# Kernel tuning notes

Measured on AMD Instinct MI355X. Metric: run time of the kernel, lower is better.

Reference implementation:

```python
import jax, jax.numpy as jnp
import numpy as np
import math

B, T, D, H, L = 64, 255, 512, 8, 8
CODEBOOK = 512
V = CODEBOOK + 3  # bos/eos/pad
COND_DIM = 512
MAX_LEN = 256
HD = D // H


def _layernorm(x, g, b, eps=1e-5):
    mu = jnp.mean(x, axis=-1, keepdims=True)
    var = jnp.mean(jnp.square(x - mu), axis=-1, keepdims=True)
    return (x - mu) * jax.lax.rsqrt(var + eps) * g + b


def setup_inputs() -> dict:
    key = jax.random.key(0)
    ks = jax.random.split(key, 24)
    s = 0.02
    d = {
        'tokens': jax.random.randint(ks[0], (B, T), 0, V),
        'cond': jax.random.normal(ks[1], (B, COND_DIM), jnp.float32),
        'emb': jax.random.normal(ks[2], (V, D), jnp.float32) * s,  # tied token_emb / head weight
        'pos_emb': jax.random.normal(ks[3], (1, MAX_LEN, D), jnp.float32) * s,
        'cond_w1': jax.random.normal(ks[4], (COND_DIM, D), jnp.float32) * s,
        'cond_b1': jnp.zeros((D,), jnp.float32),
        'cond_w2': jax.random.normal(ks[5], (D, D), jnp.float32) * s,
        'cond_b2': jnp.zeros((D,), jnp.float32),
        'ln1_g': jnp.ones((L, D), jnp.float32),
        'ln1_b': jnp.zeros((L, D), jnp.float32),
        'qkv_w': jax.random.normal(ks[6], (L, D, 3 * D), jnp.float32) * s,
        'qkv_b': jnp.zeros((L, 3 * D), jnp.float32),
        'proj_w': jax.random.normal(ks[7], (L, D, D), jnp.float32) * s,
        'proj_b': jnp.zeros((L, D), jnp.float32),
        'ln2_g': jnp.ones((L, D), jnp.float32),
        'ln2_b': jnp.zeros((L, D), jnp.float32),
        'mlp_w1': jax.random.normal(ks[8], (L, D, 4 * D), jnp.float32) * s,
        'mlp_b1': jnp.zeros((L, 4 * D), jnp.float32),
        'mlp_w2': jax.random.normal(ks[9], (L, 4 * D, D), jnp.float32) * s,
        'mlp_b2': jnp.zeros((L, D), jnp.float32),
        'lnf_g': jnp.ones((D,), jnp.float32),
        'lnf_b': jnp.zeros((D,), jnp.float32),
    }
    return d


def reference(tokens, cond, emb, pos_emb, cond_w1, cond_b1, cond_w2, cond_b2,
              ln1_g, ln1_b, qkv_w, qkv_b, proj_w, proj_b,
              ln2_g, ln2_b, mlp_w1, mlp_b1, mlp_w2, mlp_b2, lnf_g, lnf_b):
    b, t = tokens.shape
    h = emb[tokens] + pos_emb[:, :t, :]                              # [B,T,D]
    c = jax.nn.silu(cond @ cond_w1 + cond_b1) @ cond_w2 + cond_b2    # [B,D]
    h = jnp.concatenate([c[:, None, :], h], axis=1)                  # [B,S,D]
    S = t + 1
    causal = jnp.tril(jnp.ones((S, S), bool))
    scale = 1.0 / math.sqrt(HD)
    for i in range(L):
        x = _layernorm(h, ln1_g[i], ln1_b[i])
        qkv = (x @ qkv_w[i] + qkv_b[i]).reshape(b, S, 3, H, HD).transpose(2, 0, 3, 1, 4)
        q, k, v = qkv[0], qkv[1], qkv[2]                             # [B,H,S,hd]
        a = jnp.einsum('bhsd,bhtd->bhst', q, k) * scale
        a = jnp.where(causal, a, -jnp.inf)
        a = jax.nn.softmax(a, axis=-1)
        o = jnp.einsum('bhst,bhtd->bhsd', a, v).transpose(0, 2, 1, 3).reshape(b, S, D)
        h = h + o @ proj_w[i] + proj_b[i]
        x = _layernorm(h, ln2_g[i], ln2_b[i])
        h = h + jax.nn.gelu(x @ mlp_w1[i] + mlp_b1[i], approximate=False) @ mlp_w2[i] + mlp_b2[i]
    h = _layernorm(h, lnf_g, lnf_b)
    return (h @ emb.T)[:, 1:, :]                                     # [B,T,V]
```

## Files before the change

### kernel.cpp

```cpp
#include <hip/hip_runtime.h>
#include <hip/hip_bf16.h>

typedef __attribute__((ext_vector_type(8))) short bf16x8;
typedef __attribute__((ext_vector_type(4))) float f32x4;
typedef __attribute__((ext_vector_type(4))) unsigned short u16x4;
typedef __attribute__((ext_vector_type(8))) unsigned short u16x8;
typedef unsigned short u16;

#define DEV static __device__ __forceinline__

DEV float bf2f(u16 u) {
  union { unsigned int i; float f; } c; c.i = ((unsigned int)u) << 16; return c.f;
}
DEV u16 f2bf(float f) {
  union { float f; unsigned int i; } c; c.f = f;
  unsigned int i = c.i;
  i += 0x7FFFu + ((i >> 16) & 1u);
  return (u16)(i >> 16);
}

DEV void gload_lds16(const void* g, void* l) {
  __builtin_amdgcn_global_load_lds((const __attribute__((address_space(1))) void*)g,
                                   (__attribute__((address_space(3))) void*)l, 16, 0, 0);
}

DEV f32x4 mfma16(bf16x8 a, bf16x8 b, f32x4 c) {
  return __builtin_amdgcn_mfma_f32_16x16x32_bf16(a, b, c, 0, 0, 0);
}

template<int N> DEV void vwait() { asm volatile("s_waitcnt vmcnt(%0)" :: "n"(N) : "memory"); }

DEV float fasterf(float x) {
  float ax = fabsf(x);
  float t = 1.0f / (1.0f + 0.3275911f * ax);
  float y = t * (0.254829592f + t * (-0.284496736f + t * (1.421413741f +
            t * (-1.453152027f + t * 1.061405429f))));
  float r = 1.0f - y * __expf(-ax * ax);
  return copysignf(r, x);
}
DEV float gelu(float v) { return 0.5f * v * (1.0f + fasterf(v * 0.70710678118f)); }

__global__ __launch_bounds__(256) void ktranspose(const float* __restrict__ in, u16* __restrict__ out,
                                                  int K, int N) {
  __shared__ u16 tile[32][33];
  const float* src = in + (size_t)blockIdx.z * K * N;
  u16* dst = out + (size_t)blockIdx.z * K * N;
  const int n0 = blockIdx.x * 32, k0 = blockIdx.y * 32;
  const int tx = threadIdx.x, ty = threadIdx.y;
#pragma unroll
  for (int i = ty; i < 32; i += 8) tile[i][tx] = f2bf(src[(size_t)(k0 + i) * N + n0 + tx]);
  __syncthreads();
#pragma unroll
  for (int i = ty; i < 32; i += 8) dst[(size_t)(n0 + i) * K + k0 + tx] = tile[tx][i];
}

__global__ __launch_bounds__(256) void kcvt(const float* __restrict__ in, u16* __restrict__ out, int n) {
  int i = blockIdx.x * 256 + threadIdx.x;
  if (i < n) out[i] = f2bf(in[i]);
}

__global__ __launch_bounds__(256) void kcond(const float* __restrict__ cond, const float* __restrict__ w1,
                                             const float* __restrict__ b1, const float* __restrict__ w2,
                                             const float* __restrict__ b2, float* __restrict__ h) {
  __shared__ float xr[512];
  __shared__ float t1[512];
  const int b = blockIdx.x, tid = threadIdx.x;
  for (int i = tid; i < 512; i += 256) xr[i] = cond[b * 512 + i];
  __syncthreads();
  for (int j = tid; j < 512; j += 256) {
    float acc = b1[j];
    for (int k = 0; k < 512; ++k) acc += xr[k] * w1[k * 512 + j];
    t1[j] = acc / (1.f + __expf(-acc));
  }
  __syncthreads();
  for (int j = tid; j < 512; j += 256) {
    float acc = b2[j];
    for (int k = 0; k < 512; ++k) acc += t1[k] * w2[k * 512 + j];
    h[(size_t)b * 256 * 512 + j] = acc;
  }
}

__global__ __launch_bounds__(256) void kembed(const int* __restrict__ tok, const float* __restrict__ emb,
                                              const float* __restrict__ pos, float* __restrict__ h) {
  const int idx = blockIdx.x;
  const int b = idx / 255, t = idx % 255;
  const int c = threadIdx.x * 2;
  const int tk = tok[idx];
  float2 ev = *(const float2*)(emb + (size_t)tk * 512 + c);
  float2 pv = *(const float2*)(pos + (size_t)t * 512 + c);
  float2 r;
  r.x = ev.x + pv.x;
  r.y = ev.y + pv.y;
  *(float2*)(h + ((size_t)b * 256 + 1 + t) * 512 + c) = r;
}

__global__ __launch_bounds__(256) void kln(const float* __restrict__ hin, const float* __restrict__ g,
                                           const float* __restrict__ bt, u16* __restrict__ out) {
  const int row = blockIdx.x * 4 + (threadIdx.x >> 6), lane = threadIdx.x & 63;
  const float4* x = (const float4*)(hin + (size_t)row * 512);
  float4 v0 = x[lane], v1 = x[lane + 64];
  float s1 = v0.x + v0.y + v0.z + v0.w + v1.x + v1.y + v1.z + v1.w;
  float s2 = v0.x * v0.x + v0.y * v0.y + v0.z * v0.z + v0.w * v0.w +
             v1.x * v1.x + v1.y * v1.y + v1.z * v1.z + v1.w * v1.w;
#pragma unroll
  for (int off = 1; off < 64; off <<= 1) { s1 += __shfl_xor(s1, off); s2 += __shfl_xor(s2, off); }
  float mu = s1 * (1.f / 512.f);
  float var = s2 * (1.f / 512.f) - mu * mu;
  float rs = rsqrtf(var + 1e-5f);
  const int c0 = lane * 4;
  float4 g0 = *(const float4*)(g + c0), g1 = *(const float4*)(g + 256 + c0);
  float4 b0 = *(const float4*)(bt + c0), b1 = *(const float4*)(bt + 256 + c0);
  u16x4 o0, o1;
  o0[0] = f2bf((v0.x - mu) * rs * g0.x + b0.x);
  o0[1] = f2bf((v0.y - mu) * rs * g0.y + b0.y);
  o0[2] = f2bf((v0.z - mu) * rs * g0.z + b0.z);
  o0[3] = f2bf((v0.w - mu) * rs * g0.w + b0.w);
  o1[0] = f2bf((v1.x - mu) * rs * g1.x + b1.x);
  o1[1] = f2bf((v1.y - mu) * rs * g1.y + b1.y);
  o1[2] = f2bf((v1.z - mu) * rs * g1.z + b1.z);
  o1[3] = f2bf((v1.w - mu) * rs * g1.w + b1.w);
  *(u16x4*)(out + (size_t)row * 512 + c0) = o0;
  *(u16x4*)(out + (size_t)row * 512 + 256 + c0) = o1;
}

template<int MODE, int FM>
__global__ __launch_bounds__(512, 2) void kgemm8(const u16* __restrict__ A, const u16* __restrict__ Bt,
                                                 const float* __restrict__ bias, void* __restrict__ Cout,
                                                 int M, int N, int K) {
  constexpr int BM = FM * 32;
  constexpr int ABYTES = BM * 128;
  constexpr int BBYTES = 256 * 128;
  constexpr int AH = ABYTES / 2, BH = BBYTES / 2;
  constexpr int ALD = AH / 8192;
  constexpr int BOFF = 2 * ABYTES;
  __shared__ __align__(16) char shm[2 * ABYTES + 2 * BBYTES];

  const int tid = threadIdx.x;
  const int lane = tid & 63;
  const int wid = tid >> 6;
  const int wr = wid >> 2;
  const int wc = wid & 3;
  const int fr = lane & 15, fq = lane >> 4;
  const int axor = (fr & 7) << 4;
  const int m0 = blockIdx.x * BM, n0 = blockIdx.y * 256;
  const int nkt = K >> 6;
  const int Kb = K * 2;
  const char* Ab = (const char*)A;
  const char* Bb = (const char*)Bt;

  unsigned aOff[2][ALD], bOff[2][2];
#pragma unroll
  for (int h = 0; h < 2; ++h) {
#pragma unroll
    for (int j = 0; j < ALD; ++j) {
      int d = h * AH + j * 8192 + tid * 16;
      int row = d >> 7, pc = (d >> 4) & 7;
      aOff[h][j] = (unsigned)((m0 + row) * Kb + ((pc ^ (row & 7)) << 4));
    }
#pragma unroll
    for (int j = 0; j < 2; ++j) {
      int d = h * BH + j * 8192 + tid * 16;
      int row = d >> 7, pc = (d >> 4) & 7;
      bOff[h][j] = (unsigned)((n0 + row) * Kb + ((pc ^ (row & 7)) << 4));
    }
  }

  auto stA = [&](int kt, int h, int b) {
#pragma unroll
    for (int j = 0; j < ALD; ++j)
      gload_lds16(Ab + (size_t)aOff[h][j] + (size_t)kt * 128,
                  shm + b * ABYTES + h * AH + j * 8192 + tid * 16);
  };
  auto stB = [&](int kt, int h, int b) {
#pragma unroll
    for (int j = 0; j < 2; ++j)
      gload_lds16(Bb + (size_t)bOff[h][j] + (size_t)kt * 128,
                  shm + BOFF + b * BBYTES + h * BH + j * 8192 + tid * 16);
  };
  auto rdA = [&](int b, int m, int ks) {
    return *(const bf16x8*)(shm + b * ABYTES + (wr * (BM / 2) + m * 16 + fr) * 128 +
                            ((ks * 64 + fq * 16) ^ axor));
  };
  auto rdB = [&](int b, int n, int ks) {
    return *(const bf16x8*)(shm + BOFF + b * BBYTES + (wc * 64 + n * 16 + fr) * 128 +
                            ((ks * 64 + fq * 16) ^ axor));
  };

  f32x4 acc[FM][4];
#pragma unroll
  for (int i = 0; i < FM; ++i)
#pragma unroll
    for (int j = 0; j < 4; ++j) acc[i][j] = f32x4{0.f, 0.f, 0.f, 0.f};

  stA(0, 0, 0); stA(0, 1, 0); stB(0, 0, 0); stB(0, 1, 0);
  if (nkt > 1) { stA(1, 0, 1); stA(1, 1, 1); }
  vwait<2 * ALD>();
  __builtin_amdgcn_sched_barrier(0);
  __builtin_amdgcn_s_barrier();

  for (int kt = 0; kt < nkt; ++kt) {
    const int cur = kt & 1;
    const bool sb = (kt + 1 < nkt);
    const bool sa = (kt + 2 < nkt);
    bf16x8 aF[FM][2], bF[4][2];
#pragma unroll
    for (int m = 0; m < FM; ++m) aF[m][0] = rdA(cur, m, 0);
#pragma unroll
    for (int n = 0; n < 4; ++n) bF[n][0] = rdB(cur, n, 0);
    if (sb) stB(kt + 1, 0, cur ^ 1);
    __builtin_amdgcn_s_barrier();
    __builtin_amdgcn_s_setprio(1);
#pragma unroll
    for (int m = 0; m < FM / 2; ++m)
#pragma unroll
      for (int n = 0; n < 4; ++n) acc[m][n] = mfma16(aF[m][0], bF[n][0], acc[m][n]);
    __builtin_amdgcn_s_setprio(0);
    __builtin_amdgcn_s_barrier();
#pragma unroll
    for (int m = 0; m < FM; ++m) aF[m][1] = rdA(cur, m, 1);
#pragma unroll
    for (int n = 0; n < 4; ++n) bF[n][1] = rdB(cur, n, 1);
    if (sb) stB(kt + 1, 1, cur ^ 1);
    __builtin_amdgcn_s_barrier();
    __builtin_amdgcn_s_setprio(1);
#pragma unroll
    for (int m = FM / 2; m < FM; ++m)
#pragma unroll
      for (int n = 0; n < 4; ++n) acc[m][n] = mfma16(aF[m][0], bF[n][0], acc[m][n]);
    __builtin_amdgcn_s_setprio(0);
    asm volatile("s_waitcnt lgkmcnt(0)" ::: "memory");
    __builtin_amdgcn_sched_barrier(0);
    __builtin_amdgcn_s_barrier();
    if (sa) stA(kt + 2, 0, cur);
    __builtin_amdgcn_s_barrier();
    __builtin_amdgcn_s_setprio(1);
#pragma unroll
    for (int m = 0; m < FM / 2; ++m)
#pragma unroll
      for (int n = 0; n < 4; ++n) acc[m][n] = mfma16(aF[m][1], bF[n][1], acc[m][n]);
    __builtin_amdgcn_s_setprio(0);
    __builtin_amdgcn_s_barrier();
    if (sa) stA(kt + 2, 1, cur);
    __builtin_amdgcn_s_barrier();
    __builtin_amdgcn_s_setprio(1);
#pragma unroll
    for (int m = FM / 2; m < FM; ++m)
#pragma unroll
      for (int n = 0; n < 4; ++n) acc[m][n] = mfma16(aF[m][1], bF[n][1], acc[m][n]);
    __builtin_amdgcn_s_setprio(0);
    if (sa) vwait<2 * ALD>(); else vwait<0>();
    __builtin_amdgcn_sched_barrier(0);
    __builtin_amdgcn_s_barrier();
  }

  float bv[4];
#pragma unroll
  for (int n = 0; n < 4; ++n) bv[n] = bias[n0 + wc * 64 + n * 16 + fr];

  if (MODE == 0 || MODE == 1) {
    u16* C = (u16*)Cout;
#pragma unroll
    for (int m = 0; m < FM; ++m)
#pragma unroll
      for (int r = 0; r < 4; ++r) {
        int row = m0 + wr * (BM / 2) + m * 16 + fq * 4 + r;
        u16* cp = C + (size_t)row * N + n0 + wc * 64 + fr;
#pragma unroll
        for (int n = 0; n < 4; ++n) {
          float v = acc[m][n][r] + bv[n];
          if (MODE == 1) v = gelu(v);
          cp[n * 16] = f2bf(v);
        }
      }
  } else {
    float* hC = (float*)Cout;
#pragma unroll
    for (int m = 0; m < FM; ++m)
#pragma unroll
      for (int r = 0; r < 4; ++r) {
        int row = m0 + wr * (BM / 2) + m * 16 + fq * 4 + r;
        float* hp = hC + (size_t)row * N + n0 + wc * 64 + fr;
#pragma unroll
        for (int n = 0; n < 4; ++n) hp[n * 16] += acc[m][n][r] + bv[n];
      }
  }
}

template<int MODE>
__global__ __launch_bounds__(256, 2) void kgemm3(const u16* __restrict__ A, const u16* __restrict__ Bt,
                                                 const float* __restrict__ bias, void* __restrict__ Cout,
                                                 int M, int N, int K) {
  __shared__ __align__(16) u16 As[3][4096];
  __shared__ __align__(16) u16 Bs[3][4096];
  const int tid = threadIdx.x;
  const int lane = tid & 63;
  const int wr = tid >> 7, wc = (tid >> 6) & 1;
  const int m0 = blockIdx.x * 128, n0 = blockIdx.y * 128;
  const int nkt = K >> 5;
  const size_t Kb = (size_t)K * 2;

  const int srow = tid >> 2;
  const int schunk = tid & 3;
  const int sc = schunk ^ ((srow >> 1) & 3);
  const int d1 = tid * 16, d2 = tid * 16 + 4096;
  int brA = n0 + srow, brB = n0 + srow + 64;
  if (MODE == 3) { brA = min(brA, N - 1); brB = min(brB, N - 1); }
  const char* Ab = (const char*)A;
  const char* Bb = (const char*)Bt;
  const size_t a0 = (size_t)(m0 + srow) * Kb + sc * 16;
  const size_t a1 = (size_t)(m0 + srow + 64) * Kb + sc * 16;
  const size_t b0 = (size_t)brA * Kb + sc * 16;
  const size_t b1 = (size_t)brB * Kb + sc * 16;

  f32x4 acc[4][4];
#pragma unroll
  for (int i = 0; i < 4; ++i)
#pragma unroll
    for (int j = 0; j < 4; ++j) acc[i][j] = f32x4{0.f, 0.f, 0.f, 0.f};

#pragma unroll
  for (int t = 0; t < 2; ++t) {
    const size_t ko = (size_t)t * 64;
    gload_lds16(Ab + a0 + ko, (char*)As[t] + d1);
    gload_lds16(Ab + a1 + ko, (char*)As[t] + d2);
    gload_lds16(Bb + b0 + ko, (char*)Bs[t] + d1);
    gload_lds16(Bb + b1 + ko, (char*)Bs[t] + d2);
  }
  asm volatile("s_waitcnt vmcnt(4)" ::: "memory");
  __builtin_amdgcn_s_barrier();
  __builtin_amdgcn_sched_barrier(0);

  const int kchunk = (((lane >> 4) ^ ((lane >> 1) & 3)) << 4);
  const int arow = wr * 64 + (lane & 15);
  const int brow = wc * 64 + (lane & 15);

  for (int kt = 0; kt < nkt; ++kt) {
    const int bufc = kt % 3;
    const bool deep = (kt + 2 < nkt);
    if (deep) {
      const int bufn = (kt + 2) % 3;
      const size_t ko = (size_t)(kt + 2) * 64;
      gload_lds16(Ab + a0 + ko, (char*)As[bufn] + d1);
      gload_lds16(Ab + a1 + ko, (char*)As[bufn] + d2);
      gload_lds16(Bb + b0 + ko, (char*)Bs[bufn] + d1);
      gload_lds16(Bb + b1 + ko, (char*)Bs[bufn] + d2);
    }
    const char* Ap = (const char*)As[bufc];
    const char* Bp = (const char*)Bs[bufc];
    bf16x8 aF[4], bF[4];
#pragma unroll
    for (int mt = 0; mt < 4; ++mt) aF[mt] = *(const bf16x8*)(Ap + (arow + mt * 16) * 64 + kchunk);
#pragma unroll
    for (int nt = 0; nt < 4; ++nt) bF[nt] = *(const bf16x8*)(Bp + (brow + nt * 16) * 64 + kchunk);
#pragma unroll
    for (int mt = 0; mt < 4; ++mt)
#pragma unroll
      for (int nt = 0; nt < 4; ++nt)
        acc[mt][nt] = mfma16(aF[mt], bF[nt], acc[mt][nt]);
    if (deep) {
      asm volatile("s_waitcnt vmcnt(4)" ::: "memory");
    } else {
      asm volatile("s_waitcnt vmcnt(0)" ::: "memory");
    }
    __builtin_amdgcn_s_barrier();
    __builtin_amdgcn_sched_barrier(0);
  }

  if (MODE == 3) {
    float* C = (float*)Cout;
#pragma unroll
    for (int mt = 0; mt < 4; ++mt)
#pragma unroll
      for (int r = 0; r < 4; ++r) {
        int row = m0 + wr * 64 + mt * 16 + (lane >> 4) * 4 + r;
        int s = row & 255;
        if (s == 0) continue;
        int bb = row >> 8;
        float* cp = C + ((size_t)bb * 255 + (s - 1)) * 515 + n0 + wc * 64 + (lane & 15);
#pragma unroll
        for (int nt = 0; nt < 4; ++nt) {
          int col = n0 + wc * 64 + nt * 16 + (lane & 15);
          if (col < 515) cp[nt * 16] = acc[mt][nt][r];
        }
      }
  }
}

__global__ __launch_bounds__(256, 1) void kattn(const u16* __restrict__ qkv, u16* __restrict__ o) {
  __shared__ __align__(16) u16 Ks[256][72];
  __shared__ __align__(16) u16 Vt[64][264];
  __shared__ __align__(16) u16 Ps[4][64][72];
  const int tid = threadIdx.x, wv = tid >> 6, lane = tid & 63;
  const int bh = blockIdx.x, bb = bh >> 3, hh = bh & 7;
  const size_t base = (size_t)bb * 256 * 1536 + hh * 64;

  for (int c = tid; c < 2048; c += 256) {
    int s = c >> 3, pp = c & 7;
    u16x8 kv = *(const u16x8*)(qkv + base + (size_t)s * 1536 + 512 + pp * 8);
    *(u16x8*)&Ks[s][pp * 8] = kv;
    u16x8 vv = *(const u16x8*)(qkv + base + (size_t)s * 1536 + 1024 + pp * 8);
#pragma unroll
    for (int j = 0; j < 8; ++j) Vt[pp * 8 + j][s] = vv[j];
  }
  __syncthreads();

  bf16x8 qf[4][2];
#pragma unroll
  for (int mt = 0; mt < 4; ++mt)
#pragma unroll
    for (int ks = 0; ks < 2; ++ks)
      qf[mt][ks] = *(const bf16x8*)(qkv + base +
                   (size_t)(wv * 64 + mt * 16 + (lane & 15)) * 1536 + ks * 32 + (lane >> 4) * 8);

  const float scale = 0.125f;
  float mrow[4][4], lsum[4][4];
#pragma unroll
  for (int mt = 0; mt < 4; ++mt)
#pragma unroll
    for (int r = 0; r < 4; ++r) { mrow[mt][r] = -1e30f; lsum[mt][r] = 0.f; }

  for (int ct = 0; ct <= wv; ++ct) {
    f32x4 sacc[4][4];
#pragma unroll
    for (int i = 0; i < 4; ++i)
#pragma unroll
      for (int j = 0; j < 4; ++j) sacc[i][j] = f32x4{0.f, 0.f, 0.f, 0.f};
#pragma unroll
    for (int ks = 0; ks < 2; ++ks) {
      bf16x8 kf[4];
#pragma unroll
      for (int nt = 0; nt < 4; ++nt)
        kf[nt] = *(const bf16x8*)&Ks[ct * 64 + nt * 16 + (lane & 15)][ks * 32 + (lane >> 4) * 8];
#pragma unroll
      for (int mt = 0; mt < 4; ++mt)
#pragma unroll
        for (int nt = 0; nt < 4; ++nt)
          sacc[mt][nt] = mfma16(qf[mt][ks], kf[nt], sacc[mt][nt]);
    }
#pragma unroll
    for (int mt = 0; mt < 4; ++mt)
#pragma unroll
      for (int r = 0; r < 4; ++r) {
        int srow = wv * 64 + mt * 16 + (lane >> 4) * 4 + r;
        float mx = -1e30f;
#pragma unroll
        for (int nt = 0; nt < 4; ++nt) {
          int tcol = ct * 64 + nt * 16 + (lane & 15);
          float v = sacc[mt][nt][r] * scale;
          if (tcol > srow) v = -1e30f;
          mx = fmaxf(mx, v);
        }
#pragma unroll
        for (int off = 1; off < 16; off <<= 1) mx = fmaxf(mx, __shfl_xor(mx, off));
        mrow[mt][r] = fmaxf(mrow[mt][r], mx);
      }
  }

  f32x4 oacc[4][4];
#pragma unroll
  for (int i = 0; i < 4; ++i)
#pragma unroll
    for (int j = 0; j < 4; ++j) oacc[i][j] = f32x4{0.f, 0.f, 0.f, 0.f};

  for (int ct = 0; ct <= wv; ++ct) {
    f32x4 sacc[4][4];
#pragma unroll
    for (int i = 0; i < 4; ++i)
#pragma unroll
      for (int j = 0; j < 4; ++j) sacc[i][j] = f32x4{0.f, 0.f, 0.f, 0.f};
#pragma unroll
    for (int ks = 0; ks < 2; ++ks) {
      bf16x8 kf[4];
#pragma unroll
      for (int nt = 0; nt < 4; ++nt)
        kf[nt] = *(const bf16x8*)&Ks[ct * 64 + nt * 16 + (lane & 15)][ks * 32 + (lane >> 4) * 8];
#pragma unroll
      for (int mt = 0; mt < 4; ++mt)
#pragma unroll
        for (int nt = 0; nt < 4; ++nt)
          sacc[mt][nt] = mfma16(qf[mt][ks], kf[nt], sacc[mt][nt]);
    }
#pragma unroll
    for (int mt = 0; mt < 4; ++mt)
#pragma unroll
      for (int r = 0; r < 4; ++r) {
        int srow = wv * 64 + mt * 16 + (lane >> 4) * 4 + r;
        float ps = 0.f;
#pragma unroll
        for (int nt = 0; nt < 4; ++nt) {
          int tcol = ct * 64 + nt * 16 + (lane & 15);
          float v = sacc[mt][nt][r] * scale;
          float pe = (tcol > srow) ? 0.f : __expf(v - mrow[mt][r]);
          ps += pe;
          Ps[wv][mt * 16 + (lane >> 4) * 4 + r][nt * 16 + (lane & 15)] = f2bf(pe);
        }
#pragma unroll
        for (int off = 1; off < 16; off <<= 1) ps += __shfl_xor(ps, off);
        lsum[mt][r] += ps;
      }
#pragma unroll
    for (int ks = 0; ks < 2; ++ks) {
      bf16x8 pf[4], vf[4];
#pragma unroll
      for (int mt = 0; mt < 4; ++mt)
        pf[mt] = *(const bf16x8*)&Ps[wv][mt * 16 + (lane & 15)][ks * 32 + (lane >> 4) * 8];
#pragma unroll
      for (int nt = 0; nt < 4; ++nt)
        vf[nt] = *(const bf16x8*)&Vt[nt * 16 + (lane & 15)][ct * 64 + ks * 32 + (lane >> 4) * 8];
#pragma unroll
      for (int mt = 0; mt < 4; ++mt)
#pragma unroll
        for (int nt = 0; nt < 4; ++nt)
          oacc[mt][nt] = mfma16(pf[mt], vf[nt], oacc[mt][nt]);
    }
  }

#pragma unroll
  for (int mt = 0; mt < 4; ++mt)
#pragma unroll
    for (int r = 0; r < 4; ++r) {
      int s = wv * 64 + mt * 16 + (lane >> 4) * 4 + r;
      float inv = 1.f / lsum[mt][r];
      u16* op = o + ((size_t)bb * 256 + s) * 512 + hh * 64 + (lane & 15);
#pragma unroll
      for (int nt = 0; nt < 4; ++nt) op[nt * 16] = f2bf(oacc[mt][nt][r] * inv);
    }
}

extern "C" void kernel_launch(void* const* d_in, const int* in_sizes, int n_in,
                              void* d_out, int out_size, void* d_ws, size_t ws_size,
                              hipStream_t stream) {
  const int* tokens = (const int*)d_in[0];
  const float* cond = (const float*)d_in[1];
  const float* emb = (const float*)d_in[2];
  const float* pos = (const float*)d_in[3];
  const float* cw1 = (const float*)d_in[4];
  const float* cb1 = (const float*)d_in[5];
  const float* cw2 = (const float*)d_in[6];
  const float* cb2 = (const float*)d_in[7];
  const float* ln1g = (const float*)d_in[8];
  const float* ln1b = (const float*)d_in[9];
  const float* qkvw = (const float*)d_in[10];
  const float* qkvb = (const float*)d_in[11];
  const float* projw = (const float*)d_in[12];
  const float* projb = (const float*)d_in[13];
  const float* ln2g = (const float*)d_in[14];
  const float* ln2b = (const float*)d_in[15];
  const float* w1 = (const float*)d_in[16];
  const float* b1 = (const float*)d_in[17];
  const float* w2 = (const float*)d_in[18];
  const float* b2 = (const float*)d_in[19];
  const float* lnfg = (const float*)d_in[20];
  const float* lnfb = (const float*)d_in[21];

  const size_t NEEDED = (size_t)16384 * 512 * 4
                      + (size_t)16384 * 512 * 2
                      + (size_t)16384 * 2048 * 2
                      + (size_t)8 * 1536 * 512 * 2
                      + (size_t)8 * 512 * 512 * 2
                      + (size_t)8 * 2048 * 512 * 2
                      + (size_t)8 * 512 * 2048 * 2;
  if (ws_size < NEEDED) return;

  char* p = (char*)d_ws;
  float* h = (float*)p;        p += (size_t)16384 * 512 * 4;
  u16* xln = (u16*)p;          p += (size_t)16384 * 512 * 2;
  u16* big = (u16*)p;          p += (size_t)16384 * 2048 * 2;
  u16* attn_o = big + (size_t)16384 * 1536;
  u16* embB = big;
  u16* qkvT = (u16*)p;         p += (size_t)8 * 1536 * 512 * 2;
  u16* projT = (u16*)p;        p += (size_t)8 * 512 * 512 * 2;
  u16* w1T = (u16*)p;          p += (size_t)8 * 2048 * 512 * 2;
  u16* w2T = (u16*)p;          p += (size_t)8 * 512 * 2048 * 2;

  ktranspose<<<dim3(48, 16, 8), dim3(32, 8), 0, stream>>>(qkvw, qkvT, 512, 1536);
  ktranspose<<<dim3(16, 16, 8), dim3(32, 8), 0, stream>>>(projw, projT, 512, 512);
  ktranspose<<<dim3(64, 16, 8), dim3(32, 8), 0, stream>>>(w1, w1T, 512, 2048);
  ktranspose<<<dim3(16, 64, 8), dim3(32, 8), 0, stream>>>(w2, w2T, 2048, 512);

  kembed<<<16320, 256, 0, stream>>>(tokens, emb, pos, h);
  kcond<<<64, 256, 0, stream>>>(cond, cw1, cb1, cw2, cb2, h);

  for (int l = 0; l < 8; ++l) {
    kln<<<4096, 256, 0, stream>>>(h, ln1g + l * 512, ln1b + l * 512, xln);
    kgemm8<0, 8><<<dim3(64, 6), 512, 0, stream>>>(xln, qkvT + (size_t)l * 1536 * 512,
                                                  qkvb + l * 1536, big, 16384, 1536, 512);
    kattn<<<512, 256, 0, stream>>>(big, attn_o);
    kgemm8<2, 4><<<dim3(128, 2), 512, 0, stream>>>(attn_o, projT + (size_t)l * 512 * 512,
                                                   projb + l * 512, h, 16384, 512, 512);
    kln<<<4096, 256, 0, stream>>>(h, ln2g + l * 512, ln2b + l * 512, xln);
    kgemm8<1, 8><<<dim3(64, 8), 512, 0, stream>>>(xln, w1T + (size_t)l * 2048 * 512,
                                                  b1 + l * 2048, big, 16384, 2048, 512);
    kgemm8<2, 4><<<dim3(128, 2), 512, 0, stream>>>(big, w2T + (size_t)l * 512 * 2048,
                                                   b2 + l * 512, h, 16384, 512, 2048);
  }
  kln<<<4096, 256, 0, stream>>>(h, lnfg, lnfb, xln);
  kcvt<<<1030, 256, 0, stream>>>(emb, embB, 515 * 512);
  kgemm3<3><<<dim3(128, 5), 256, 0, stream>>>(xln, embB, nullptr, d_out, 16384, 515, 512);
}
```

Before: 1.973 ms.

## Use 128x128 gemm for QKV/MLP1, one-pass online-softmax attention, tanh GELU

Switches the QKV and MLP-up GEMMs from the large 256x256-tile kgemm8 to the smaller 128x128 triple-buffered kgemm3, which is extended with bias and GELU epilogues, and leaves kgemm8 handling only the residual-add case. Attention drops its separate max pass and uses an online softmax that rescales the running sum and output accumulator, so QK^T is computed once instead of twice. GELU becomes the tanh approximation, which is cheaper per element but deviates from the exact erf GELU in the reference.

```diff
diff --git a/kernel.cpp b/kernel.cpp
--- a/kernel.cpp
+++ b/kernel.cpp
@@ -30,15 +30,12 @@
 
 template<int N> DEV void vwait() { asm volatile("s_waitcnt vmcnt(%0)" :: "n"(N) : "memory"); }
 
-DEV float fasterf(float x) {
-  float ax = fabsf(x);
-  float t = 1.0f / (1.0f + 0.3275911f * ax);
-  float y = t * (0.254829592f + t * (-0.284496736f + t * (1.421413741f +
-            t * (-1.453152027f + t * 1.061405429f))));
-  float r = 1.0f - y * __expf(-ax * ax);
-  return copysignf(r, x);
-}
-DEV float gelu(float v) { return 0.5f * v * (1.0f + fasterf(v * 0.70710678118f)); }
+DEV float gelu(float x) {
+  float t2 = __builtin_fmaf(0.044715f * x * x, x, x);
+  float e = __expf(1.5957691216f * t2);
+  float th = 1.f - 2.f / (e + 1.f);
+  return 0.5f * x * (1.f + th);
+}
 
 __global__ __launch_bounds__(256) void ktranspose(const float* __restrict__ in, u16* __restrict__ out,
                                                   int K, int N) {
@@ -123,6 +120,139 @@
   *(u16x4*)(out + (size_t)row * 512 + 256 + c0) = o1;
 }
 
+template<int MODE>
+__global__ __launch_bounds__(256, 2) void kgemm3(const u16* __restrict__ A, const u16* __restrict__ Bt,
+                                                 const float* __restrict__ bias, void* __restrict__ Cout,
+                                                 int M, int N, int K) {
+  __shared__ __align__(16) u16 As[3][4096];
+  __shared__ __align__(16) u16 Bs[3][4096];
+  const int tid = threadIdx.x;
+  const int lane = tid & 63;
+  const int wr = tid >> 7, wc = (tid >> 6) & 1;
+  const int m0 = blockIdx.x * 128, n0 = blockIdx.y * 128;
+  const int nkt = K >> 5;
+  const size_t Kb = (size_t)K * 2;
+
+  const int srow = tid >> 2;
+  const int schunk = tid & 3;
+  const int sc = schunk ^ ((srow >> 1) & 3);
+  const int d1 = tid * 16, d2 = tid * 16 + 4096;
+  int brA = n0 + srow, brB = n0 + srow + 64;
+  if (MODE == 3) { brA = min(brA, N - 1); brB = min(brB, N - 1); }
+  const char* Ab = (const char*)A;
+  const char* Bb = (const char*)Bt;
+  const size_t a0 = (size_t)(m0 + srow) * Kb + sc * 16;
+  const size_t a1 = (size_t)(m0 + srow + 64) * Kb + sc * 16;
+  const size_t b0 = (size_t)brA * Kb + sc * 16;
+  const size_t b1 = (size_t)brB * Kb + sc * 16;
+
+  f32x4 acc[4][4];
+#pragma unroll
+  for (int i = 0; i < 4; ++i)
+#pragma unroll
+    for (int j = 0; j < 4; ++j) acc[i][j] = f32x4{0.f, 0.f, 0.f, 0.f};
+
+#pragma unroll
+  for (int t = 0; t < 2; ++t) {
+    const size_t ko = (size_t)t * 64;
+    gload_lds16(Ab + a0 + ko, (char*)As[t] + d1);
+    gload_lds16(Ab + a1 + ko, (char*)As[t] + d2);
+    gload_lds16(Bb + b0 + ko, (char*)Bs[t] + d1);
+    gload_lds16(Bb + b1 + ko, (char*)Bs[t] + d2);
+  }
+  asm volatile("s_waitcnt vmcnt(4)" ::: "memory");
+  __builtin_amdgcn_s_barrier();
+  __builtin_amdgcn_sched_barrier(0);
+
+  const int kchunk = (((lane >> 4) ^ ((lane >> 1) & 3)) << 4);
+  const int arow = wr * 64 + (lane & 15);
+  const int brow = wc * 64 + (lane & 15);
+
+  for (int kt = 0; kt < nkt; ++kt) {
+    const int bufc = kt % 3;
+    const bool deep = (kt + 2 < nkt);
+    if (deep) {
+      const int bufn = (kt + 2) % 3;
+      const size_t ko = (size_t)(kt + 2) * 64;
+      gload_lds16(Ab + a0 + ko, (char*)As[bufn] + d1);
+      gload_lds16(Ab + a1 + ko, (char*)As[bufn] + d2);
+      gload_lds16(Bb + b0 + ko, (char*)Bs[bufn] + d1);
+      gload_lds16(Bb + b1 + ko, (char*)Bs[bufn] + d2);
+    }
+    const char* Ap = (const char*)As[bufc];
+    const char* Bp = (const char*)Bs[bufc];
+    bf16x8 aF[4], bF[4];
+#pragma unroll
+    for (int mt = 0; mt < 4; ++mt) aF[mt] = *(const bf16x8*)(Ap + (arow + mt * 16) * 64 + kchunk);
+#pragma unroll
+    for (int nt = 0; nt < 4; ++nt) bF[nt] = *(const bf16x8*)(Bp + (brow + nt * 16) * 64 + kchunk);
+#pragma unroll
+    for (int mt = 0; mt < 4; ++mt)
+#pragma unroll
+      for (int nt = 0; nt < 4; ++nt)
+        acc[mt][nt] = mfma16(aF[mt], bF[nt], acc[mt][nt]);
+    if (deep) {
+      asm volatile("s_waitcnt vmcnt(4)" ::: "memory");
+    } else {
+      asm volatile("s_waitcnt vmcnt(0)" ::: "memory");
+    }
+    __builtin_amdgcn_s_barrier();
+    __builtin_amdgcn_sched_barrier(0);
+  }
+
+  float bv[4];
+#pragma unroll
+  for (int nt = 0; nt < 4; ++nt) {
+    int col = n0 + wc * 64 + nt * 16 + (lane & 15);
+    bv[nt] = (MODE == 3) ? 0.f : bias[col];
+  }
+
+  if (MODE == 0 || MODE == 1) {
+    u16* C = (u16*)Cout;
+#pragma unroll
+    for (int mt = 0; mt < 4; ++mt)
+#pragma unroll
+      for (int r = 0; r < 4; ++r) {
+        int row = m0 + wr * 64 + mt * 16 + (lane >> 4) * 4 + r;
+        u16* cp = C + (size_t)row * N + n0 + wc * 64 + (lane & 15);
+#pragma unroll
+        for (int nt = 0; nt < 4; ++nt) {
+          float v = acc[mt][nt][r] + bv[nt];
+          if (MODE == 1) v = gelu(v);
+          cp[nt * 16] = f2bf(v);
+        }
+      }
+  } else if (MODE == 2) {
+    float* hC = (float*)Cout;
+#pragma unroll
+    for (int mt = 0; mt < 4; ++mt)
+#pragma unroll
+      for (int r = 0; r < 4; ++r) {
+        int row = m0 + wr * 64 + mt * 16 + (lane >> 4) * 4 + r;
+        float* hp = hC + (size_t)row * N + n0 + wc * 64 + (lane & 15);
+#pragma unroll
+        for (int nt = 0; nt < 4; ++nt) hp[nt * 16] += acc[mt][nt][r] + bv[nt];
+      }
+  } else {
+    float* C = (float*)Cout;
+#pragma unroll
+    for (int mt = 0; mt < 4; ++mt)
+#pragma unroll
+      for (int r = 0; r < 4; ++r) {
+        int row = m0 + wr * 64 + mt * 16 + (lane >> 4) * 4 + r;
+        int s = row & 255;
+        if (s == 0) continue;
+        int bb = row >> 8;
+        float* cp = C + ((size_t)bb * 255 + (s - 1)) * 515 + n0 + wc * 64 + (lane & 15);
+#pragma unroll
+        for (int nt = 0; nt < 4; ++nt) {
+          int col = n0 + wc * 64 + nt * 16 + (lane & 15);
+          if (col < 515) cp[nt * 16] = acc[mt][nt][r];
+        }
+      }
+  }
+}
+
 template<int MODE, int FM>
 __global__ __launch_bounds__(512, 2) void kgemm8(const u16* __restrict__ A, const u16* __restrict__ Bt,
                                                  const float* __restrict__ bias, void* __restrict__ Cout,
@@ -257,133 +387,16 @@
 #pragma unroll
   for (int n = 0; n < 4; ++n) bv[n] = bias[n0 + wc * 64 + n * 16 + fr];
 
-  if (MODE == 0 || MODE == 1) {
-    u16* C = (u16*)Cout;
-#pragma unroll
-    for (int m = 0; m < FM; ++m)
-#pragma unroll
-      for (int r = 0; r < 4; ++r) {
-        int row = m0 + wr * (BM / 2) + m * 16 + fq * 4 + r;
-        u16* cp = C + (size_t)row * N + n0 + wc * 64 + fr;
-#pragma unroll
-        for (int n = 0; n < 4; ++n) {
-          float v = acc[m][n][r] + bv[n];
-          if (MODE == 1) v = gelu(v);
-          cp[n * 16] = f2bf(v);
-        }
-      }
-  } else {
-    float* hC = (float*)Cout;
-#pragma unroll
-    for (int m = 0; m < FM; ++m)
-#pragma unroll
-      for (int r = 0; r < 4; ++r) {
-        int row = m0 + wr * (BM / 2) + m * 16 + fq * 4 + r;
-        float* hp = hC + (size_t)row * N + n0 + wc * 64 + fr;
-#pragma unroll
-        for (int n = 0; n < 4; ++n) hp[n * 16] += acc[m][n][r] + bv[n];
-      }
-  }
-}
-
-template<int MODE>
-__global__ __launch_bounds__(256, 2) void kgemm3(const u16* __restrict__ A, const u16* __restrict__ Bt,
-                                                 const float* __restrict__ bias, void* __restrict__ Cout,
-                                                 int M, int N, int K) {
-  __shared__ __align__(16) u16 As[3][4096];
-  __shared__ __align__(16) u16 Bs[3][4096];
-  const int tid = threadIdx.x;
-  const int lane = tid & 63;
-  const int wr = tid >> 7, wc = (tid >> 6) & 1;
-  const int m0 = blockIdx.x * 128, n0 = blockIdx.y * 128;
-  const int nkt = K >> 5;
-  const size_t Kb = (size_t)K * 2;
-
-  const int srow = tid >> 2;
-  const int schunk = tid & 3;
-  const int sc = schunk ^ ((srow >> 1) & 3);
-  const int d1 = tid * 16, d2 = tid * 16 + 4096;
-  int brA = n0 + srow, brB = n0 + srow + 64;
-  if (MODE == 3) { brA = min(brA, N - 1); brB = min(brB, N - 1); }
-  const char* Ab = (const char*)A;
-  const char* Bb = (const char*)Bt;
-  const size_t a0 = (size_t)(m0 + srow) * Kb + sc * 16;
-  const size_t a1 = (size_t)(m0 + srow + 64) * Kb + sc * 16;
-  const size_t b0 = (size_t)brA * Kb + sc * 16;
-  const size_t b1 = (size_t)brB * Kb + sc * 16;
-
-  f32x4 acc[4][4];
-#pragma unroll
-  for (int i = 0; i < 4; ++i)
-#pragma unroll
-    for (int j = 0; j < 4; ++j) acc[i][j] = f32x4{0.f, 0.f, 0.f, 0.f};
-
-#pragma unroll
-  for (int t = 0; t < 2; ++t) {
-    const size_t ko = (size_t)t * 64;
-    gload_lds16(Ab + a0 + ko, (char*)As[t] + d1);
-    gload_lds16(Ab + a1 + ko, (char*)As[t] + d2);
-    gload_lds16(Bb + b0 + ko, (char*)Bs[t] + d1);
-    gload_lds16(Bb + b1 + ko, (char*)Bs[t] + d2);
-  }
-  asm volatile("s_waitcnt vmcnt(4)" ::: "memory");
-  __builtin_amdgcn_s_barrier();
-  __builtin_amdgcn_sched_barrier(0);
-
-  const int kchunk = (((lane >> 4) ^ ((lane >> 1) & 3)) << 4);
-  const int arow = wr * 64 + (lane & 15);
-  const int brow = wc * 64 + (lane & 15);
-
-  for (int kt = 0; kt < nkt; ++kt) {
-    const int bufc = kt % 3;
-    const bool deep = (kt + 2 < nkt);
-    if (deep) {
-      const int bufn = (kt + 2) % 3;
-      const size_t ko = (size_t)(kt + 2) * 64;
-      gload_lds16(Ab + a0 + ko, (char*)As[bufn] + d1);
-      gload_lds16(Ab + a1 + ko, (char*)As[bufn] + d2);
-      gload_lds16(Bb + b0 + ko, (char*)Bs[bufn] + d1);
-      gload_lds16(Bb + b1 + ko, (char*)Bs[bufn] + d2);
-    }
-    const char* Ap = (const char*)As[bufc];
-    const char* Bp = (const char*)Bs[bufc];
-    bf16x8 aF[4], bF[4];
-#pragma unroll
-    for (int mt = 0; mt < 4; ++mt) aF[mt] = *(const bf16x8*)(Ap + (arow + mt * 16) * 64 + kchunk);
-#pragma unroll
-    for (int nt = 0; nt < 4; ++nt) bF[nt] = *(const bf16x8*)(Bp + (brow + nt * 16) * 64 + kchunk);
-#pragma unroll
-    for (int mt = 0; mt < 4; ++mt)
-#pragma unroll
-      for (int nt = 0; nt < 4; ++nt)
-        acc[mt][nt] = mfma16(aF[mt], bF[nt], acc[mt][nt]);
-    if (deep) {
-      asm volatile("s_waitcnt vmcnt(4)" ::: "memory");
-    } else {
-      asm volatile("s_waitcnt vmcnt(0)" ::: "memory");
-    }
-    __builtin_amdgcn_s_barrier();
-    __builtin_amdgcn_sched_barrier(0);
-  }
-
-  if (MODE == 3) {
-    float* C = (float*)Cout;
-#pragma unroll
-    for (int mt = 0; mt < 4; ++mt)
-#pragma unroll
-      for (int r = 0; r < 4; ++r) {
-        int row = m0 + wr * 64 + mt * 16 + (lane >> 4) * 4 + r;
-        int s = row & 255;
-        if (s == 0) continue;
-        int bb = row >> 8;
-        float* cp = C + ((size_t)bb * 255 + (s - 1)) * 515 + n0 + wc * 64 + (lane & 15);
-#pragma unroll
-        for (int nt = 0; nt < 4; ++nt) {
-          int col = n0 + wc * 64 + nt * 16 + (lane & 15);
-          if (col < 515) cp[nt * 16] = acc[mt][nt][r];
-        }
-      }
-  }
+  float* hC = (float*)Cout;
+#pragma unroll
+  for (int m = 0; m < FM; ++m)
+#pragma unroll
+    for (int r = 0; r < 4; ++r) {
+      int row = m0 + wr * (BM / 2) + m * 16 + fq * 4 + r;
+      float* hp = hC + (size_t)row * N + n0 + wc * 64 + fr;
+#pragma unroll
+      for (int n = 0; n < 4; ++n) hp[n * 16] += acc[m][n][r] + bv[n];
+    }
 }
 
 __global__ __launch_bounds__(256, 1) void kattn(const u16* __restrict__ qkv, u16* __restrict__ o) {
@@ -419,6 +432,12 @@
 #pragma unroll
     for (int r = 0; r < 4; ++r) { mrow[mt][r] = -1e30f; lsum[mt][r] = 0.f; }
 
+  f32x4 oacc[4][4];
+#pragma unroll
+  for (int i = 0; i < 4; ++i)
+#pragma unroll
+    for (int j = 0; j < 4; ++j) oacc[i][j] = f32x4{0.f, 0.f, 0.f, 0.f};
+
   for (int ct = 0; ct <= wv; ++ct) {
     f32x4 sacc[4][4];
 #pragma unroll
@@ -442,61 +461,32 @@
 #pragma unroll
       for (int r = 0; r < 4; ++r) {
         int srow = wv * 64 + mt * 16 + (lane >> 4) * 4 + r;
+        float v[4];
         float mx = -1e30f;
 #pragma unroll
         for (int nt = 0; nt < 4; ++nt) {
           int tcol = ct * 64 + nt * 16 + (lane & 15);
-          float v = sacc[mt][nt][r] * scale;
-          if (tcol > srow) v = -1e30f;
-          mx = fmaxf(mx, v);
+          float vv = sacc[mt][nt][r] * scale;
+          v[nt] = (tcol > srow) ? -1e30f : vv;
+          mx = fmaxf(mx, v[nt]);
         }
 #pragma unroll
         for (int off = 1; off < 16; off <<= 1) mx = fmaxf(mx, __shfl_xor(mx, off));
-        mrow[mt][r] = fmaxf(mrow[mt][r], mx);
-      }
-  }
-
-  f32x4 oacc[4][4];
-#pragma unroll
-  for (int i = 0; i < 4; ++i)
-#pragma unroll
-    for (int j = 0; j < 4; ++j) oacc[i][j] = f32x4{0.f, 0.f, 0.f, 0.f};
-
-  for (int ct = 0; ct <= wv; ++ct) {
-    f32x4 sacc[4][4];
-#pragma unroll
-    for (int i = 0; i < 4; ++i)
-#pragma unroll
-      for (int j = 0; j < 4; ++j) sacc[i][j] = f32x4{0.f, 0.f, 0.f, 0.f};
-#pragma unroll
-    for (int ks = 0; ks < 2; ++ks) {
-      bf16x8 kf[4];
-#pragma unroll
-      for (int nt = 0; nt < 4; ++nt)
-        kf[nt] = *(const bf16x8*)&Ks[ct * 64 + nt * 16 + (lane & 15)][ks * 32 + (lane >> 4) * 8];
-#pragma unroll
-      for (int mt = 0; mt < 4; ++mt)
-#pragma unroll
-        for (int nt = 0; nt < 4; ++nt)
-          sacc[mt][nt] = mfma16(qf[mt][ks], kf[nt], sacc[mt][nt]);
-    }
-#pragma unroll
-    for (int mt = 0; mt < 4; ++mt)
-#pragma unroll
-      for (int r = 0; r < 4; ++r) {
-        int srow = wv * 64 + mt * 16 + (lane >> 4) * 4 + r;
+        float mnew = fmaxf(mrow[mt][r], mx);
+        float sf = __expf(mrow[mt][r] - mnew);
+        mrow[mt][r] = mnew;
         float ps = 0.f;
 #pragma unroll
         for (int nt = 0; nt < 4; ++nt) {
-          int tcol = ct * 64 + nt * 16 + (lane & 15);
-          float v = sacc[mt][nt][r] * scale;
-          float pe = (tcol > srow) ? 0.f : __expf(v - mrow[mt][r]);
+          float pe = (v[nt] <= -1e29f) ? 0.f : __expf(v[nt] - mnew);
           ps += pe;
           Ps[wv][mt * 16 + (lane >> 4) * 4 + r][nt * 16 + (lane & 15)] = f2bf(pe);
         }
 #pragma unroll
         for (int off = 1; off < 16; off <<= 1) ps += __shfl_xor(ps, off);
-        lsum[mt][r] += ps;
+        lsum[mt][r] = lsum[mt][r] * sf + ps;
+#pragma unroll
+        for (int nt = 0; nt < 4; ++nt) oacc[mt][nt][r] *= sf;
       }
 #pragma unroll
     for (int ks = 0; ks < 2; ++ks) {
@@ -583,14 +573,14 @@
 
   for (int l = 0; l < 8; ++l) {
     kln<<<4096, 256, 0, stream>>>(h, ln1g + l * 512, ln1b + l * 512, xln);
-    kgemm8<0, 8><<<dim3(64, 6), 512, 0, stream>>>(xln, qkvT + (size_t)l * 1536 * 512,
-                                                  qkvb + l * 1536, big, 16384, 1536, 512);
+    kgemm3<0><<<dim3(128, 12), 256, 0, stream>>>(xln, qkvT + (size_t)l * 1536 * 512,
+                                                 qkvb + l * 1536, big, 16384, 1536, 512);
     kattn<<<512, 256, 0, stream>>>(big, attn_o);
     kgemm8<2, 4><<<dim3(128, 2), 512, 0, stream>>>(attn_o, projT + (size_t)l * 512 * 512,
                                                    projb + l * 512, h, 16384, 512, 512);
     kln<<<4096, 256, 0, stream>>>(h, ln2g + l * 512, ln2b + l * 512, xln);
-    kgemm8<1, 8><<<dim3(64, 8), 512, 0, stream>>>(xln, w1T + (size_t)l * 2048 * 512,
-                                                  b1 + l * 2048, big, 16384, 2048, 512);
+    kgemm3<1><<<dim3(128, 16), 256, 0, stream>>>(xln, w1T + (size_t)l * 2048 * 512,
+                                                 b1 + l * 2048, big, 16384, 2048, 512);
     kgemm8<2, 4><<<dim3(128, 2), 512, 0, stream>>>(big, w2T + (size_t)l * 512 * 2048,
                                                    b2 + l * 512, h, 16384, 512, 2048);
   }
```

Result: no change. 1.985 ms (+0.6%).
